# Performance work log

Measured on AMD Instinct MI355X. Metric: run time of the kernel, lower is better.

## Reference

```python
import jax, jax.numpy as jnp
import numpy as np

B, S, D = 4, 2048, 1024


def setup_inputs() -> dict:
    key = jax.random.key(0)
    ks = jax.random.split(key, 4)
    scale = 1.0 / np.sqrt(D)
    x = jax.random.normal(ks[0], (B, S, D), dtype=jnp.float32)
    Wk = jax.random.normal(ks[1], (D, D), dtype=jnp.float32) * scale
    Wq = jax.random.normal(ks[2], (D, D), dtype=jnp.float32) * scale
    Wv = jax.random.normal(ks[3], (D, D), dtype=jnp.float32) * scale
    bk = jnp.zeros((D,), dtype=jnp.float32)
    bq = jnp.zeros((D,), dtype=jnp.float32)
    bv = jnp.zeros((D,), dtype=jnp.float32)
    return {"x": x, "Wk": Wk, "bk": bk, "Wq": Wq, "bq": bq,
            "Wv": Wv, "bv": bv, "dims": 2}


def correlated_weight(k, q, v, dims):
    # correlation between every query position and every key position,
    # scaled by sqrt(d) for numerical stability (standard correlation attn)
    d = q.shape[-1]
    scores = jnp.einsum("bqd,bkd->bqk", q, k) / jnp.sqrt(jnp.asarray(d, q.dtype))
    w = jax.nn.softmax(scores, axis=dims)          # [B, S, S]
    return jnp.einsum("bqk,bkd->bqd", w, v)        # [B, S, D]


def reference(x, Wk, bk, Wq, bq, Wv, bv, dims):
    # injected key/query/value funcs instantiated as Linear layers
    k = jnp.einsum("bsd,de->bse", x, Wk) + bk
    q = jnp.einsum("bsd,de->bse", x, Wq) + bq
    v = jnp.einsum("bsd,de->bse", x, Wv) + bv
    return correlated_weight(k, q, v, dims)
```

## Files before the change

### kernel.cpp

```cpp
#include <hip/hip_runtime.h>
#include <hip/hip_bf16.h>
#include <stdint.h>


typedef unsigned short u16;
typedef __bf16 bf16x8 __attribute__((ext_vector_type(8)));
typedef float  f32x4  __attribute__((ext_vector_type(4)));
typedef float  f32x16 __attribute__((ext_vector_type(16)));
typedef u16    u16x4  __attribute__((ext_vector_type(4)));
typedef u16    u16x8  __attribute__((ext_vector_type(8)));

__device__ __forceinline__ u16 f2bf(float f) {
  union { float f; uint32_t u; } v; v.f = f;
  uint32_t r = v.u + 0x7fffu + ((v.u >> 16) & 1u);
  return (u16)(r >> 16);
}
__device__ __forceinline__ float bf2f(u16 b) {
  union { uint32_t u; float f; } v; v.u = (uint32_t)b << 16; return v.f;
}

#define GLD_LDS16(gp, lp) __builtin_amdgcn_global_load_lds(                   \
    (const __attribute__((address_space(1))) void*)(gp),                      \
    (__attribute__((address_space(3))) void*)(lp), 16, 0, 0)


__global__ __launch_bounds__(256)
void prep_all(const float* __restrict__ x,
              const float* __restrict__ Wq, const float* __restrict__ Wk,
              const float* __restrict__ Wv,
              const float* __restrict__ bq, const float* __restrict__ bk,
              const float* __restrict__ bv,
              u16* __restrict__ xb, u16* __restrict__ wt,
              float* __restrict__ bc) {
  __shared__ float t[32][33];
  const int bid = blockIdx.x;
  if (bid < 4096) {
    int i = (bid * 256 + threadIdx.x) * 8;
    float4 v0 = *(const float4*)(x + i);
    float4 v1 = *(const float4*)(x + i + 4);
    u16x8 o;
    o[0] = f2bf(v0.x); o[1] = f2bf(v0.y); o[2] = f2bf(v0.z); o[3] = f2bf(v0.w);
    o[4] = f2bf(v1.x); o[5] = f2bf(v1.y); o[6] = f2bf(v1.z); o[7] = f2bf(v1.w);
    *(u16x8*)(xb + i) = o;
  } else if (bid < 4096 + 3072) {
    int b2 = bid - 4096;
    int z = b2 >> 10, rem = b2 & 1023;
    int e0 = (rem & 31) * 32, d0 = (rem >> 5) * 32;
    const float* W = z == 0 ? Wq : (z == 1 ? Wk : Wv);
    u16* dst = wt + (size_t)z * 1024 * 1024;
    int tx = threadIdx.x & 31, ty = threadIdx.x >> 5;
    #pragma unroll
    for (int i = 0; i < 4; ++i)
      t[ty + i * 8][tx] = W[(size_t)(d0 + ty + i * 8) * 1024 + e0 + tx];
    __syncthreads();
    #pragma unroll
    for (int i = 0; i < 4; ++i)
      dst[(size_t)(e0 + ty + i * 8) * 1024 + d0 + tx] =
          f2bf(t[tx][ty + i * 8]);
  } else {
    int i = (bid - 7168) * 256 + threadIdx.x;
    if (i < 3072)
      bc[i] = (i < 1024) ? bq[i] : (i < 2048 ? bk[i - 1024] : bv[i - 2048]);
  }
}


__global__ __launch_bounds__(256)
void gemm_qkv(const u16* __restrict__ A, int lda,
              const u16* __restrict__ B, int ldb,
              u16* __restrict__ C, int ldc,
              const float* __restrict__ bias, int K,
              u16* __restrict__ vTp) {
  __shared__ __align__(16) u16 smem[128 * 132];
  u16* As = smem;
  u16* Bs = smem + 8192;
  const int lane = threadIdx.x & 63;
  const int wv = threadIdx.x >> 6;

  const u16* Ab = A + (size_t)blockIdx.y * 128 * lda;
  const u16* Bb = B + (size_t)blockIdx.x * 128 * ldb;

  const int srow = lane >> 3;
  const int scol = ((lane & 7) ^ (lane >> 3)) * 8;
  const int r32 = lane & 31;
  const int half = lane >> 5;
  const int rx = lane & 7;
  const int wm = (wv >> 1) * 64;
  const int wn = (wv & 1) * 64;

  f32x16 acc[2][2];
  #pragma unroll
  for (int i = 0; i < 2; ++i)
    #pragma unroll
    for (int j = 0; j < 2; ++j) acc[i][j] = (f32x16)0.0f;

  for (int k0 = 0; k0 < K; k0 += 64) {
    #pragma unroll
    for (int i = 0; i < 4; ++i) {
      int r = wv * 32 + i * 8;
      GLD_LDS16(Ab + (size_t)(r + srow) * lda + k0 + scol, As + r * 64);
      GLD_LDS16(Bb + (size_t)(r + srow) * ldb + k0 + scol, Bs + r * 64);
    }
    __syncthreads();

    bf16x8 af[2][4], bfr[2][4];
    #pragma unroll
    for (int i = 0; i < 2; ++i)
      #pragma unroll
      for (int t = 0; t < 4; ++t) {
        int pc = ((t * 2 + half) ^ rx) * 8;
        af[i][t]  = *(const bf16x8*)(As + (wm + i * 32 + r32) * 64 + pc);
        bfr[i][t] = *(const bf16x8*)(Bs + (wn + i * 32 + r32) * 64 + pc);
      }
    #pragma unroll
    for (int i = 0; i < 2; ++i)
      #pragma unroll
      for (int j = 0; j < 2; ++j)
        #pragma unroll
        for (int t = 0; t < 4; ++t)
          acc[i][j] = __builtin_amdgcn_mfma_f32_32x32x16_bf16(
              af[i][t], bfr[j][t], acc[i][j], 0, 0, 0);
    __syncthreads();
  }

  if (blockIdx.x < 16) {
    const int ccol0 = blockIdx.x * 128 + wn + r32;
    const int crow0 = blockIdx.y * 128 + wm + 4 * half;
    #pragma unroll
    for (int i = 0; i < 2; ++i) {
      #pragma unroll
      for (int e = 0; e < 16; ++e) {
        int m = crow0 + i * 32 + (e & 3) + 8 * (e >> 2);
        #pragma unroll
        for (int j = 0; j < 2; ++j) {
          int n = ccol0 + j * 32;
          C[(size_t)m * ldc + n] = f2bf(acc[i][j][e] + bias[n]);
        }
      }
    }
  } else {
    u16 (*t)[132] = (u16(*)[132])smem;
    #pragma unroll
    for (int i = 0; i < 2; ++i) {
      #pragma unroll
      for (int j = 0; j < 2; ++j) {
        const int nl = wn + j * 32 + r32;
        const float bv = bias[blockIdx.x * 128 + nl];
        #pragma unroll
        for (int eg = 0; eg < 4; ++eg) {
          const int mb = wm + i * 32 + 4 * half + 8 * eg;
          u16x4 o;
          #pragma unroll
          for (int q = 0; q < 4; ++q) o[q] = f2bf(acc[i][j][eg * 4 + q] + bv);
          *(u16x4*)&t[nl][mb] = o;
        }
      }
    }
    __syncthreads();
    const int tid = threadIdx.x;
    const int bb = blockIdx.y >> 4;
    const int s0 = (blockIdx.y & 15) * 128 + (tid & 15) * 8;
    const int e_base = (blockIdx.x - 16) * 128;
    u16* dstb = vTp + (size_t)bb * 1024 * 2048;
    #pragma unroll
    for (int p = 0; p < 8; ++p) {
      const int el = (tid >> 4) + p * 16;
      u16x8 o;
      #pragma unroll
      for (int q = 0; q < 8; ++q) o[q] = t[el][(tid & 15) * 8 + q];
      *(u16x8*)(dstb + (size_t)(e_base + el) * 2048 + s0) = o;
    }
  }
}


#define FENCE8 asm volatile("" ::: "memory")
#define BARR8  do { FENCE8; __builtin_amdgcn_s_barrier(); FENCE8; } while (0)
#define WAITL8 asm volatile("s_waitcnt lgkmcnt(0)" ::: "memory")
#define VMW(N) asm volatile("s_waitcnt vmcnt(" #N ")" ::: "memory")

#define STAGE_A8(S, H, TT) do {                                               \
    GLD_LDS16(pA[H][0] + (TT) * 64,                                           \
              As + (S) * 16384 + ((H) * 64 + wv * 8) * 64);                   \
    GLD_LDS16(pA[H][1] + (TT) * 64,                                           \
              As + (S) * 16384 + ((H) * 64 + 128 + wv * 8) * 64);             \
  } while (0)

#define STAGE_B8(S, H, TT) do {                                               \
    GLD_LDS16(pB[H][0] + (TT) * 64,                                           \
              Bs + (S) * 16384 + ((H) * 32 + (wv >> 2) * 64 + (wv & 3) * 8) * 64); \
    GLD_LDS16(pB[H][1] + (TT) * 64,                                           \
              Bs + (S) * 16384 + ((H) * 32 + 128 + (wv >> 2) * 64 + (wv & 3) * 8) * 64); \
  } while (0)

#define RD_A8(S, MH) do {                                                     \
    _Pragma("unroll")                                                         \
    for (int mf = 0; mf < 4; ++mf) {                                          \
      const u16* p_ = As + (S) * 16384 + rdA + ((MH) * 64 + mf * 16) * 64;    \
      a[mf][0] = *(const bf16x8*)(p_ + pos0);                                 \
      a[mf][1] = *(const bf16x8*)(p_ + pos1);                                 \
    }                                                                         \
  } while (0)

#define RD_B8(S, NH) do {                                                     \
    _Pragma("unroll")                                                         \
    for (int nf = 0; nf < 2; ++nf) {                                          \
      const u16* p_ = Bs + (S) * 16384 + rdB + ((NH) * 32 + nf * 16) * 64;    \
      b[nf][0] = *(const bf16x8*)(p_ + pos0);                                 \
      b[nf][1] = *(const bf16x8*)(p_ + pos1);                                 \
    }                                                                         \
  } while (0)

#define MFMA_Q8(MH, NH) do {                                                  \
    _Pragma("unroll")                                                         \
    for (int ks = 0; ks < 2; ++ks)                                            \
      _Pragma("unroll")                                                       \
      for (int mf = 0; mf < 4; ++mf)                                          \
        _Pragma("unroll")                                                     \
        for (int nf = 0; nf < 2; ++nf)                                        \
          acc[(MH) * 4 + mf][(NH) * 2 + nf] =                                 \
              __builtin_amdgcn_mfma_f32_16x16x32_bf16(                        \
                  a[mf][ks], b[nf][ks], acc[(MH) * 4 + mf][(NH) * 2 + nf],    \
                  0, 0, 0);                                                   \
  } while (0)

#define GROUP8(S, T, EN1, EN2, WAITST) do {                                   \
    RD_A8(S, 0); RD_B8(S, 0);                                                 \
    if (EN1) STAGE_B8((S) ^ 1, 0, (T) + 1);                                   \
    BARR8; WAITL8;                                                            \
    __builtin_amdgcn_s_setprio(1); MFMA_Q8(0, 0);                             \
    __builtin_amdgcn_s_setprio(0); BARR8;                                     \
    RD_B8(S, 1);                                                              \
    if (EN2) STAGE_A8(S, 0, (T) + 2);                                         \
    BARR8; WAITL8;                                                            \
    __builtin_amdgcn_s_setprio(1); MFMA_Q8(0, 1);                             \
    __builtin_amdgcn_s_setprio(0); BARR8;                                     \
    RD_A8(S, 1);                                                              \
    if (EN2) STAGE_B8(S, 1, (T) + 2);                                         \
    BARR8; WAITL8;                                                            \
    __builtin_amdgcn_s_setprio(1); MFMA_Q8(1, 1);                             \
    __builtin_amdgcn_s_setprio(0); BARR8;                                     \
    RD_B8(S, 0);                                                              \
    if (EN2) STAGE_A8(S, 1, (T) + 2);                                         \
    BARR8; WAITL8;                                                            \
    __builtin_amdgcn_s_setprio(1); MFMA_Q8(1, 0);                             \
    __builtin_amdgcn_s_setprio(0); WAITST; BARR8;                             \
  } while (0)

template <int NT>
__global__ __launch_bounds__(512)
void gemm8p(const u16* __restrict__ A, int lda, long long sA,
            const u16* __restrict__ B, int ldb, long long sB,
            u16* __restrict__ C, int ldc, long long sC, float scale) {
  __shared__ __align__(16) u16 As[2 * 256 * 64];
  __shared__ __align__(16) u16 Bs[2 * 256 * 64];

  const int lane = threadIdx.x & 63;
  const int wv   = threadIdx.x >> 6;
  const int wm   = wv >> 2;
  const int wn   = wv & 3;
  const int l15  = lane & 15;
  const int hi4  = lane >> 4;
  const int rx7  = lane & 7;
  const int srow = lane >> 3;
  const int scem = ((lane & 7) ^ srow) * 8;

  const int nx = gridDim.x;
  const int flat = blockIdx.y * nx + blockIdx.x;
  const int nwg = nx * gridDim.y;
  const int cpx = nwg >> 3;
  const int swz = (flat & 7) * cpx + (flat >> 3);
  const int bx = swz % nx, by = swz / nx;

  const u16* Ab = A + (size_t)blockIdx.z * sA + (size_t)by * 256 * lda;
  const u16* Bb = B + (size_t)blockIdx.z * sB + (size_t)bx * 256 * ldb;

  const u16* pA[2][2];
  const u16* pB[2][2];
  #pragma unroll
  for (int h = 0; h < 2; ++h)
    #pragma unroll
    for (int r = 0; r < 2; ++r) {
      pA[h][r] = Ab + (size_t)(h * 64 + r * 128 + wv * 8 + srow) * lda + scem;
      pB[h][r] = Bb + (size_t)(h * 32 + r * 128 + (wv >> 2) * 64 +
                               (wv & 3) * 8 + srow) * ldb + scem;
    }

  const int rdA = (wm * 128 + l15) * 64;
  const int rdB = (wn * 64 + l15) * 64;
  const int pos0 = (hi4 ^ rx7) * 8;
  const int pos1 = ((4 + hi4) ^ rx7) * 8;

  f32x4 acc[8][4];
  #pragma unroll
  for (int i = 0; i < 8; ++i)
    #pragma unroll
    for (int j = 0; j < 4; ++j) acc[i][j] = (f32x4)0.0f;

  bf16x8 a[4][2], b[2][2];

  STAGE_A8(0, 0, 0); STAGE_B8(0, 1, 0); STAGE_A8(0, 1, 0); STAGE_B8(0, 0, 0);
  VMW(4);
  STAGE_A8(1, 0, 1); STAGE_B8(1, 1, 1); STAGE_A8(1, 1, 1);
  VMW(6);
  BARR8;

  #pragma unroll 1
  for (int i = 0; i < NT / 2 - 1; ++i) {
    const int t0 = 2 * i;
    GROUP8(0, t0,     1, 1, VMW(6));
    GROUP8(1, t0 + 1, 1, 1, VMW(6));
  }
  GROUP8(0, NT - 2, 1, 0, VMW(0));
  GROUP8(1, NT - 1, 0, 0, (void)0);

  const int m0 = by * 256 + wm * 128;
  const int n0 = bx * 256 + wn * 64;
  u16* Cb = C + (size_t)blockIdx.z * sC;
  #pragma unroll
  for (int fm = 0; fm < 8; ++fm) {
    const int mb = m0 + (fm >> 2) * 64 + (fm & 3) * 16 + hi4 * 4;
    #pragma unroll
    for (int e = 0; e < 4; ++e) {
      const int m = mb + e;
      #pragma unroll
      for (int fn = 0; fn < 4; ++fn) {
        const int n = n0 + (fn >> 1) * 32 + (fn & 1) * 16 + l15;
        Cb[(size_t)m * ldc + n] = f2bf(acc[fm][fn][e] * scale);
      }
    }
  }
}

__global__ __launch_bounds__(512)
void gemm_bt8(const u16* __restrict__ A, int lda, long long sA,
              const u16* __restrict__ B, int ldb, long long sB,
              float* __restrict__ C, int ldc, long long sC,
              int K, float scale) {
  __shared__ u16 As[128 * 64];
  __shared__ u16 Bs[128 * 64];
  const int lane = threadIdx.x & 63;
  const int wv = threadIdx.x >> 6;

  const u16* Ab = A + (size_t)blockIdx.z * sA + (size_t)blockIdx.y * 128 * lda;
  const u16* Bb = B + (size_t)blockIdx.z * sB + (size_t)blockIdx.x * 128 * ldb;

  const int srow = lane >> 3;
  const int scol = ((lane & 7) ^ (lane >> 3)) * 8;
  const int r32 = lane & 31;
  const int half = lane >> 5;
  const int rx = lane & 7;
  const int wm = (wv >> 2) * 64;
  const int wn = (wv & 3) * 32;

  f32x16 acc[2];
  acc[0] = (f32x16)0.0f; acc[1] = (f32x16)0.0f;

  for (int k0 = 0; k0 < K; k0 += 64) {
    #pragma unroll
    for (int i = 0; i < 2; ++i) {
      int r = wv * 16 + i * 8;
      GLD_LDS16(Ab + (size_t)(r + srow) * lda + k0 + scol, As + r * 64);
      GLD_LDS16(Bb + (size_t)(r + srow) * ldb + k0 + scol, Bs + r * 64);
    }
    __syncthreads();

    bf16x8 af[2][4], bfr[4];
    #pragma unroll
    for (int t = 0; t < 4; ++t) {
      int pc = ((t * 2 + half) ^ rx) * 8;
      af[0][t] = *(const bf16x8*)(As + (wm + r32) * 64 + pc);
      af[1][t] = *(const bf16x8*)(As + (wm + 32 + r32) * 64 + pc);
      bfr[t]   = *(const bf16x8*)(Bs + (wn + r32) * 64 + pc);
    }
    #pragma unroll
    for (int i = 0; i < 2; ++i)
      #pragma unroll
      for (int t = 0; t < 4; ++t)
        acc[i] = __builtin_amdgcn_mfma_f32_32x32x16_bf16(
            af[i][t], bfr[t], acc[i], 0, 0, 0);
    __syncthreads();
  }

  const int ccol = blockIdx.x * 128 + wn + r32;
  const int crow0 = blockIdx.y * 128 + wm + 4 * half;
  float* Cf = C + (size_t)blockIdx.z * sC;
  #pragma unroll
  for (int i = 0; i < 2; ++i)
    #pragma unroll
    for (int e = 0; e < 16; ++e) {
      int m = crow0 + i * 32 + (e & 3) + 8 * (e >> 2);
      Cf[(size_t)m * ldc + ccol] = acc[i][e] * scale;
    }
}


__global__ __launch_bounds__(256) void softmax_rows(u16* __restrict__ P) {
  __shared__ float red[4];
  const int t = threadIdx.x;
  const int lane = t & 63, wv = t >> 6;
  u16* row = P + (size_t)blockIdx.x * 2048;
  u16x8 w = ((const u16x8*)row)[t];
  float v[8];
  #pragma unroll
  for (int j = 0; j < 8; ++j) v[j] = bf2f(w[j]);
  float m = v[0];
  #pragma unroll
  for (int j = 1; j < 8; ++j) m = fmaxf(m, v[j]);
  #pragma unroll
  for (int off = 32; off > 0; off >>= 1) m = fmaxf(m, __shfl_down(m, off));
  if (lane == 0) red[wv] = m;
  __syncthreads();
  m = fmaxf(fmaxf(red[0], red[1]), fmaxf(red[2], red[3]));
  __syncthreads();
  float e[8], s = 0.f;
  #pragma unroll
  for (int j = 0; j < 8; ++j) { e[j] = exp2f((v[j] - m) * 1.44269504f); s += e[j]; }
  #pragma unroll
  for (int off = 32; off > 0; off >>= 1) s += __shfl_down(s, off);
  if (lane == 0) red[wv] = s;
  __syncthreads();
  s = red[0] + red[1] + red[2] + red[3];
  float inv = 1.0f / s;
  u16x8 o;
  #pragma unroll
  for (int j = 0; j < 8; ++j) o[j] = f2bf(e[j] * inv);
  ((u16x8*)row)[t] = o;
}


extern "C" void kernel_launch(void* const* d_in, const int* in_sizes, int n_in,
                              void* d_out, int out_size, void* d_ws, size_t ws_size,
                              hipStream_t stream) {
  const float* x  = (const float*)d_in[0];
  const float* Wk = (const float*)d_in[1];
  const float* bk = (const float*)d_in[2];
  const float* Wq = (const float*)d_in[3];
  const float* bq = (const float*)d_in[4];
  const float* Wv = (const float*)d_in[5];
  const float* bv = (const float*)d_in[6];
  float* out = (float*)d_out;

  char* ws = (char*)d_ws;
  u16*   xb  = (u16*)(ws + 0);
  u16*   wt  = (u16*)(ws + 16777216);
  float* bc  = (float*)(ws + 23068672);
  u16*   qkv = (u16*)(ws + 23080960);
  u16*   vT  = (u16*)(ws + 73412608);
  u16*   P   = (u16*)(ws + 90189824);
  (void)in_sizes; (void)n_in; (void)out_size; (void)ws_size;

  prep_all<<<7180, 256, 0, stream>>>(x, Wq, Wk, Wv, bq, bk, bv, xb, wt, bc);

  gemm_qkv<<<dim3(24, 64, 1), 256, 0, stream>>>(
      xb, 1024, wt, 1024, qkv, 3072, bc, 1024, vT);

  gemm8p<16><<<dim3(8, 8, 4), 512, 0, stream>>>(
      qkv, 3072, 2048LL * 3072, qkv + 1024, 3072, 2048LL * 3072,
      P, 2048, 2048LL * 2048, 0.03125f);

  softmax_rows<<<8192, 256, 0, stream>>>(P);

  gemm_bt8<<<dim3(8, 16, 4), 512, 0, stream>>>(
      P, 2048, 2048LL * 2048, vT, 2048, 1024LL * 2048,
      out, 1024, 2048LL * 1024, 2048, 1.0f);
}
```

Baseline: 262.8 us.

## Use pipelined 256-tile GEMM for QK projection and PV, swizzle V GEMM blocks

The fused QKV projection is split. Q and K are now produced by the pipelined 256x256 gemm8p kernel, templated with a bias and bf16 output, and V by a dedicated transposing kernel with a block swizzle. The final P·V GEMM moves from a simple non-pipelined 128x128 kernel to a new double-buffered 128x256 kernel with 16x16x32 MFMAs, prioritised MFMA phases and block-index swizzling. The aim is better data reuse and overlap of loads with compute in the two largest GEMMs. The cost is an extra kernel launch and more complex barrier and waitcnt sequencing.

```diff
diff --git a/kernel.cpp b/kernel.cpp
--- a/kernel.cpp
+++ b/kernel.cpp
@@ -66,19 +66,22 @@
 
 
 __global__ __launch_bounds__(256)
-void gemm_qkv(const u16* __restrict__ A, int lda,
-              const u16* __restrict__ B, int ldb,
-              u16* __restrict__ C, int ldc,
-              const float* __restrict__ bias, int K,
-              u16* __restrict__ vTp) {
+void gemm_v(const u16* __restrict__ A, int lda,
+            const u16* __restrict__ B, int ldb,
+            const float* __restrict__ bias, int K,
+            u16* __restrict__ vTp) {
   __shared__ __align__(16) u16 smem[128 * 132];
   u16* As = smem;
   u16* Bs = smem + 8192;
   const int lane = threadIdx.x & 63;
   const int wv = threadIdx.x >> 6;
 
-  const u16* Ab = A + (size_t)blockIdx.y * 128 * lda;
-  const u16* Bb = B + (size_t)blockIdx.x * 128 * ldb;
+  const int flat = blockIdx.y * 8 + blockIdx.x;
+  const int swz = (flat & 7) * 64 + (flat >> 3);
+  const int bx = swz & 7, by = swz >> 3;
+
+  const u16* Ab = A + (size_t)by * 128 * lda;
+  const u16* Bb = B + (size_t)bx * 128 * ldb;
 
   const int srow = lane >> 3;
   const int scol = ((lane & 7) ^ (lane >> 3)) * 8;
@@ -123,53 +126,36 @@
     __syncthreads();
   }
 
-  if (blockIdx.x < 16) {
-    const int ccol0 = blockIdx.x * 128 + wn + r32;
-    const int crow0 = blockIdx.y * 128 + wm + 4 * half;
-    #pragma unroll
-    for (int i = 0; i < 2; ++i) {
+  u16 (*t)[132] = (u16(*)[132])smem;
+  #pragma unroll
+  for (int i = 0; i < 2; ++i) {
+    #pragma unroll
+    for (int j = 0; j < 2; ++j) {
+      const int nl = wn + j * 32 + r32;
+      const float bvv = bias[bx * 128 + nl];
       #pragma unroll
-      for (int e = 0; e < 16; ++e) {
-        int m = crow0 + i * 32 + (e & 3) + 8 * (e >> 2);
+      for (int eg = 0; eg < 4; ++eg) {
+        const int mb = wm + i * 32 + 4 * half + 8 * eg;
+        u16x4 o;
         #pragma unroll
-        for (int j = 0; j < 2; ++j) {
-          int n = ccol0 + j * 32;
-          C[(size_t)m * ldc + n] = f2bf(acc[i][j][e] + bias[n]);
-        }
+        for (int q = 0; q < 4; ++q) o[q] = f2bf(acc[i][j][eg * 4 + q] + bvv);
+        *(u16x4*)&t[nl][mb] = o;
       }
     }
-  } else {
-    u16 (*t)[132] = (u16(*)[132])smem;
-    #pragma unroll
-    for (int i = 0; i < 2; ++i) {
-      #pragma unroll
-      for (int j = 0; j < 2; ++j) {
-        const int nl = wn + j * 32 + r32;
-        const float bv = bias[blockIdx.x * 128 + nl];
-        #pragma unroll
-        for (int eg = 0; eg < 4; ++eg) {
-          const int mb = wm + i * 32 + 4 * half + 8 * eg;
-          u16x4 o;
-          #pragma unroll
-          for (int q = 0; q < 4; ++q) o[q] = f2bf(acc[i][j][eg * 4 + q] + bv);
-          *(u16x4*)&t[nl][mb] = o;
-        }
-      }
-    }
-    __syncthreads();
-    const int tid = threadIdx.x;
-    const int bb = blockIdx.y >> 4;
-    const int s0 = (blockIdx.y & 15) * 128 + (tid & 15) * 8;
-    const int e_base = (blockIdx.x - 16) * 128;
-    u16* dstb = vTp + (size_t)bb * 1024 * 2048;
-    #pragma unroll
-    for (int p = 0; p < 8; ++p) {
-      const int el = (tid >> 4) + p * 16;
-      u16x8 o;
-      #pragma unroll
-      for (int q = 0; q < 8; ++q) o[q] = t[el][(tid & 15) * 8 + q];
-      *(u16x8*)(dstb + (size_t)(e_base + el) * 2048 + s0) = o;
-    }
+  }
+  __syncthreads();
+  const int tid = threadIdx.x;
+  const int bb = by >> 4;
+  const int s0 = (by & 15) * 128 + (tid & 15) * 8;
+  const int e_base = bx * 128;
+  u16* dstb = vTp + (size_t)bb * 1024 * 2048;
+  #pragma unroll
+  for (int p = 0; p < 8; ++p) {
+    const int el = (tid >> 4) + p * 16;
+    u16x8 o;
+    #pragma unroll
+    for (int q = 0; q < 8; ++q) o[q] = t[el][(tid & 15) * 8 + q];
+    *(u16x8*)(dstb + (size_t)(e_base + el) * 2048 + s0) = o;
   }
 }
 
@@ -247,11 +233,12 @@
     __builtin_amdgcn_s_setprio(0); WAITST; BARR8;                             \
   } while (0)
 
-template <int NT>
+template <int NT, bool OUT_BF16, bool BIAS>
 __global__ __launch_bounds__(512)
 void gemm8p(const u16* __restrict__ A, int lda, long long sA,
             const u16* __restrict__ B, int ldb, long long sB,
-            u16* __restrict__ C, int ldc, long long sC, float scale) {
+            void* __restrict__ C, int ldc, long long sC,
+            const float* __restrict__ bias, float scale) {
   __shared__ __align__(16) u16 As[2 * 256 * 64];
   __shared__ __align__(16) u16 Bs[2 * 256 * 64];
 
@@ -316,7 +303,14 @@
 
   const int m0 = by * 256 + wm * 128;
   const int n0 = bx * 256 + wn * 64;
-  u16* Cb = C + (size_t)blockIdx.z * sC;
+  u16* Cb = (u16*)C + (size_t)blockIdx.z * sC;
+  float* Cf = (float*)C + (size_t)blockIdx.z * sC;
+  float bb[4];
+  if (BIAS) {
+    #pragma unroll
+    for (int fn = 0; fn < 4; ++fn)
+      bb[fn] = bias[n0 + (fn >> 1) * 32 + (fn & 1) * 16 + l15];
+  }
   #pragma unroll
   for (int fm = 0; fm < 8; ++fm) {
     const int mb = m0 + (fm >> 2) * 64 + (fm & 3) * 16 + hi4 * 4;
@@ -326,72 +320,145 @@
       #pragma unroll
       for (int fn = 0; fn < 4; ++fn) {
         const int n = n0 + (fn >> 1) * 32 + (fn & 1) * 16 + l15;
-        Cb[(size_t)m * ldc + n] = f2bf(acc[fm][fn][e] * scale);
+        float v = acc[fm][fn][e] * scale;
+        if (BIAS) v += bb[fn];
+        if (OUT_BF16) Cb[(size_t)m * ldc + n] = f2bf(v);
+        else          Cf[(size_t)m * ldc + n] = v;
       }
     }
   }
 }
 
+
+#define STAGE_AV(S, H, TT) do {                                               \
+    GLD_LDS16(pA[H] + (TT) * 64,                                              \
+              As + (S) * 8192 + ((H) * 32 + (wv >> 2) * 64 + (wv & 3) * 8) * 64); \
+  } while (0)
+
+#define RD_AV(S, MH) do {                                                     \
+    _Pragma("unroll")                                                         \
+    for (int mf = 0; mf < 2; ++mf) {                                          \
+      const u16* p_ = As + (S) * 8192 + rdA + ((MH) * 32 + mf * 16) * 64;     \
+      a[mf][0] = *(const bf16x8*)(p_ + pos0);                                 \
+      a[mf][1] = *(const bf16x8*)(p_ + pos1);                                 \
+    }                                                                         \
+  } while (0)
+
+#define MFMA_QV(MH, NH) do {                                                  \
+    _Pragma("unroll")                                                         \
+    for (int ks = 0; ks < 2; ++ks)                                            \
+      _Pragma("unroll")                                                       \
+      for (int mf = 0; mf < 2; ++mf)                                          \
+        _Pragma("unroll")                                                     \
+        for (int nf = 0; nf < 2; ++nf)                                        \
+          acc[(MH) * 2 + mf][(NH) * 2 + nf] =                                 \
+              __builtin_amdgcn_mfma_f32_16x16x32_bf16(                        \
+                  a[mf][ks], b[nf][ks], acc[(MH) * 2 + mf][(NH) * 2 + nf],    \
+                  0, 0, 0);                                                   \
+  } while (0)
+
+#define GROUPV(S, T, EN1, EN2, WAITST) do {                                   \
+    RD_AV(S, 0); RD_B8(S, 0);                                                 \
+    if (EN1) STAGE_B8((S) ^ 1, 0, (T) + 1);                                   \
+    BARR8; WAITL8;                                                            \
+    __builtin_amdgcn_s_setprio(1); MFMA_QV(0, 0);                             \
+    __builtin_amdgcn_s_setprio(0); BARR8;                                     \
+    RD_B8(S, 1);                                                              \
+    if (EN2) STAGE_AV(S, 0, (T) + 2);                                         \
+    BARR8; WAITL8;                                                            \
+    __builtin_amdgcn_s_setprio(1); MFMA_QV(0, 1);                             \
+    __builtin_amdgcn_s_setprio(0); BARR8;                                     \
+    RD_AV(S, 1);                                                              \
+    if (EN2) STAGE_B8(S, 1, (T) + 2);                                         \
+    BARR8; WAITL8;                                                            \
+    __builtin_amdgcn_s_setprio(1); MFMA_QV(1, 1);                             \
+    __builtin_amdgcn_s_setprio(0); BARR8;                                     \
+    RD_B8(S, 0);                                                              \
+    if (EN2) STAGE_AV(S, 1, (T) + 2);                                         \
+    BARR8; WAITL8;                                                            \
+    __builtin_amdgcn_s_setprio(1); MFMA_QV(1, 0);                             \
+    __builtin_amdgcn_s_setprio(0); WAITST; BARR8;                             \
+  } while (0)
+
+template <int NT>
 __global__ __launch_bounds__(512)
-void gemm_bt8(const u16* __restrict__ A, int lda, long long sA,
-              const u16* __restrict__ B, int ldb, long long sB,
-              float* __restrict__ C, int ldc, long long sC,
-              int K, float scale) {
-  __shared__ u16 As[128 * 64];
-  __shared__ u16 Bs[128 * 64];
+void gemm8pv(const u16* __restrict__ A, int lda, long long sA,
+             const u16* __restrict__ B, int ldb, long long sB,
+             float* __restrict__ C, int ldc, long long sC, float scale) {
+  __shared__ __align__(16) u16 As[2 * 128 * 64];
+  __shared__ __align__(16) u16 Bs[2 * 256 * 64];
+
   const int lane = threadIdx.x & 63;
-  const int wv = threadIdx.x >> 6;
-
-  const u16* Ab = A + (size_t)blockIdx.z * sA + (size_t)blockIdx.y * 128 * lda;
-  const u16* Bb = B + (size_t)blockIdx.z * sB + (size_t)blockIdx.x * 128 * ldb;
-
+  const int wv   = threadIdx.x >> 6;
+  const int wm   = wv >> 2;
+  const int wn   = wv & 3;
+  const int l15  = lane & 15;
+  const int hi4  = lane >> 4;
+  const int rx7  = lane & 7;
   const int srow = lane >> 3;
-  const int scol = ((lane & 7) ^ (lane >> 3)) * 8;
-  const int r32 = lane & 31;
-  const int half = lane >> 5;
-  const int rx = lane & 7;
-  const int wm = (wv >> 2) * 64;
-  const int wn = (wv & 3) * 32;
-
-  f32x16 acc[2];
-  acc[0] = (f32x16)0.0f; acc[1] = (f32x16)0.0f;
-
-  for (int k0 = 0; k0 < K; k0 += 64) {
-    #pragma unroll
-    for (int i = 0; i < 2; ++i) {
-      int r = wv * 16 + i * 8;
-      GLD_LDS16(Ab + (size_t)(r + srow) * lda + k0 + scol, As + r * 64);
-      GLD_LDS16(Bb + (size_t)(r + srow) * ldb + k0 + scol, Bs + r * 64);
+  const int scem = ((lane & 7) ^ srow) * 8;
+
+  const int flat = (blockIdx.z * gridDim.y + blockIdx.y) * gridDim.x + blockIdx.x;
+  const int swz = (flat & 7) * 32 + (flat >> 3);
+  const int bx = swz & 3, by = (swz >> 2) & 15, bz = swz >> 6;
+
+  const u16* Ab = A + (size_t)bz * sA + (size_t)by * 128 * lda;
+  const u16* Bb = B + (size_t)bz * sB + (size_t)bx * 256 * ldb;
+
+  const u16* pA[2];
+  const u16* pB[2][2];
+  #pragma unroll
+  for (int h = 0; h < 2; ++h) {
+    pA[h] = Ab + (size_t)(h * 32 + (wv >> 2) * 64 + (wv & 3) * 8 + srow) * lda + scem;
+    #pragma unroll
+    for (int r = 0; r < 2; ++r)
+      pB[h][r] = Bb + (size_t)(h * 32 + r * 128 + (wv >> 2) * 64 +
+                               (wv & 3) * 8 + srow) * ldb + scem;
+  }
+
+  const int rdA = (wm * 64 + l15) * 64;
+  const int rdB = (wn * 64 + l15) * 64;
+  const int pos0 = (hi4 ^ rx7) * 8;
+  const int pos1 = ((4 + hi4) ^ rx7) * 8;
+
+  f32x4 acc[4][4];
+  #pragma unroll
+  for (int i = 0; i < 4; ++i)
+    #pragma unroll
+    for (int j = 0; j < 4; ++j) acc[i][j] = (f32x4)0.0f;
+
+  bf16x8 a[2][2], b[2][2];
+
+  STAGE_AV(0, 0, 0); STAGE_B8(0, 1, 0); STAGE_AV(0, 1, 0); STAGE_B8(0, 0, 0);
+  STAGE_AV(1, 0, 1); STAGE_B8(1, 1, 1); STAGE_AV(1, 1, 1);
+  VMW(4);
+  BARR8;
+
+  #pragma unroll 1
+  for (int i = 0; i < NT / 2 - 1; ++i) {
+    const int t0 = 2 * i;
+    GROUPV(0, t0,     1, 1, VMW(4));
+    GROUPV(1, t0 + 1, 1, 1, VMW(4));
+  }
+  GROUPV(0, NT - 2, 1, 0, VMW(0));
+  GROUPV(1, NT - 1, 0, 0, (void)0);
+
+  float* Cf = C + (size_t)bz * sC;
+  const int m0 = by * 128 + wm * 64 + hi4 * 4;
+  const int n0 = bx * 256 + wn * 64;
+  #pragma unroll
+  for (int am = 0; am < 4; ++am) {
+    const int mb = m0 + (am >> 1) * 32 + (am & 1) * 16;
+    #pragma unroll
+    for (int e = 0; e < 4; ++e) {
+      const int m = mb + e;
+      #pragma unroll
+      for (int an = 0; an < 4; ++an) {
+        const int n = n0 + (an >> 1) * 32 + (an & 1) * 16 + l15;
+        Cf[(size_t)m * ldc + n] = acc[am][an][e] * scale;
+      }
     }
-    __syncthreads();
-
-    bf16x8 af[2][4], bfr[4];
-    #pragma unroll
-    for (int t = 0; t < 4; ++t) {
-      int pc = ((t * 2 + half) ^ rx) * 8;
-      af[0][t] = *(const bf16x8*)(As + (wm + r32) * 64 + pc);
-      af[1][t] = *(const bf16x8*)(As + (wm + 32 + r32) * 64 + pc);
-      bfr[t]   = *(const bf16x8*)(Bs + (wn + r32) * 64 + pc);
-    }
-    #pragma unroll
-    for (int i = 0; i < 2; ++i)
-      #pragma unroll
-      for (int t = 0; t < 4; ++t)
-        acc[i] = __builtin_amdgcn_mfma_f32_32x32x16_bf16(
-            af[i][t], bfr[t], acc[i], 0, 0, 0);
-    __syncthreads();
-  }
-
-  const int ccol = blockIdx.x * 128 + wn + r32;
-  const int crow0 = blockIdx.y * 128 + wm + 4 * half;
-  float* Cf = C + (size_t)blockIdx.z * sC;
-  #pragma unroll
-  for (int i = 0; i < 2; ++i)
-    #pragma unroll
-    for (int e = 0; e < 16; ++e) {
-      int m = crow0 + i * 32 + (e & 3) + 8 * (e >> 2);
-      Cf[(size_t)m * ldc + ccol] = acc[i][e] * scale;
-    }
+  }
 }
 
 
@@ -445,23 +512,26 @@
   u16*   xb  = (u16*)(ws + 0);
   u16*   wt  = (u16*)(ws + 16777216);
   float* bc  = (float*)(ws + 23068672);
-  u16*   qkv = (u16*)(ws + 23080960);
-  u16*   vT  = (u16*)(ws + 73412608);
-  u16*   P   = (u16*)(ws + 90189824);
+  u16*   qk  = (u16*)(ws + 23080960);
+  u16*   vT  = (u16*)(ws + 56635392);
+  u16*   P   = (u16*)(ws + 73412608);
   (void)in_sizes; (void)n_in; (void)out_size; (void)ws_size;
 
   prep_all<<<7180, 256, 0, stream>>>(x, Wq, Wk, Wv, bq, bk, bv, xb, wt, bc);
 
-  gemm_qkv<<<dim3(24, 64, 1), 256, 0, stream>>>(
-      xb, 1024, wt, 1024, qkv, 3072, bc, 1024, vT);
-
-  gemm8p<16><<<dim3(8, 8, 4), 512, 0, stream>>>(
-      qkv, 3072, 2048LL * 3072, qkv + 1024, 3072, 2048LL * 3072,
-      P, 2048, 2048LL * 2048, 0.03125f);
+  gemm8p<16, true, true><<<dim3(8, 32, 1), 512, 0, stream>>>(
+      xb, 1024, 0LL, wt, 1024, 0LL, (void*)qk, 2048, 0LL, bc, 1.0f);
+
+  gemm_v<<<dim3(8, 64, 1), 256, 0, stream>>>(
+      xb, 1024, wt + 2048 * 1024, 1024, bc + 2048, 1024, vT);
+
+  gemm8p<16, true, false><<<dim3(8, 8, 4), 512, 0, stream>>>(
+      qk, 2048, 2048LL * 2048, qk + 1024, 2048, 2048LL * 2048,
+      (void*)P, 2048, 2048LL * 2048, nullptr, 0.03125f);
 
   softmax_rows<<<8192, 256, 0, stream>>>(P);
 
-  gemm_bt8<<<dim3(8, 16, 4), 512, 0, stream>>>(
+  gemm8pv<32><<<dim3(4, 16, 4), 512, 0, stream>>>(
       P, 2048, 2048LL * 2048, vT, 2048, 1024LL * 2048,
-      out, 1024, 2048LL * 1024, 2048, 1.0f);
-}
+      out, 1024, 2048LL * 1024, 1.0f);
+}
```

Result: slower. 273.1 us (+3.9%).

## Split QKV projection: Q/K via pipelined 256-tile GEMM, V via swizzled transpose kernel

Applied to the files above, without the earlier changes.

The fused QKV projection kernel is split in two. Q and K are now computed by the pipelined 256x256-tile gemm8p kernel, extended with a bias add and templated output type, writing a compact [8192,2048] QK buffer. V keeps the older 128-tile kernel with its transposed write, now with a grouped block-index swizzle for cache locality. The aim is to run most of the projection FLOPs on the faster, more deeply pipelined kernel, at the cost of one extra launch and two dependent kernels.

```diff
diff --git a/kernel.cpp b/kernel.cpp
--- a/kernel.cpp
+++ b/kernel.cpp
@@ -66,19 +66,22 @@
 
 
 __global__ __launch_bounds__(256)
-void gemm_qkv(const u16* __restrict__ A, int lda,
-              const u16* __restrict__ B, int ldb,
-              u16* __restrict__ C, int ldc,
-              const float* __restrict__ bias, int K,
-              u16* __restrict__ vTp) {
+void gemm_v(const u16* __restrict__ A, int lda,
+            const u16* __restrict__ B, int ldb,
+            const float* __restrict__ bias, int K,
+            u16* __restrict__ vTp) {
   __shared__ __align__(16) u16 smem[128 * 132];
   u16* As = smem;
   u16* Bs = smem + 8192;
   const int lane = threadIdx.x & 63;
   const int wv = threadIdx.x >> 6;
 
-  const u16* Ab = A + (size_t)blockIdx.y * 128 * lda;
-  const u16* Bb = B + (size_t)blockIdx.x * 128 * ldb;
+  const int flat = blockIdx.y * 8 + blockIdx.x;
+  const int swz = (flat & 7) * 64 + (flat >> 3);
+  const int bx = swz & 7, by = swz >> 3;
+
+  const u16* Ab = A + (size_t)by * 128 * lda;
+  const u16* Bb = B + (size_t)bx * 128 * ldb;
 
   const int srow = lane >> 3;
   const int scol = ((lane & 7) ^ (lane >> 3)) * 8;
@@ -123,53 +126,36 @@
     __syncthreads();
   }
 
-  if (blockIdx.x < 16) {
-    const int ccol0 = blockIdx.x * 128 + wn + r32;
-    const int crow0 = blockIdx.y * 128 + wm + 4 * half;
-    #pragma unroll
-    for (int i = 0; i < 2; ++i) {
+  u16 (*t)[132] = (u16(*)[132])smem;
+  #pragma unroll
+  for (int i = 0; i < 2; ++i) {
+    #pragma unroll
+    for (int j = 0; j < 2; ++j) {
+      const int nl = wn + j * 32 + r32;
+      const float bvv = bias[bx * 128 + nl];
       #pragma unroll
-      for (int e = 0; e < 16; ++e) {
-        int m = crow0 + i * 32 + (e & 3) + 8 * (e >> 2);
+      for (int eg = 0; eg < 4; ++eg) {
+        const int mb = wm + i * 32 + 4 * half + 8 * eg;
+        u16x4 o;
         #pragma unroll
-        for (int j = 0; j < 2; ++j) {
-          int n = ccol0 + j * 32;
-          C[(size_t)m * ldc + n] = f2bf(acc[i][j][e] + bias[n]);
-        }
+        for (int q = 0; q < 4; ++q) o[q] = f2bf(acc[i][j][eg * 4 + q] + bvv);
+        *(u16x4*)&t[nl][mb] = o;
       }
     }
-  } else {
-    u16 (*t)[132] = (u16(*)[132])smem;
-    #pragma unroll
-    for (int i = 0; i < 2; ++i) {
-      #pragma unroll
-      for (int j = 0; j < 2; ++j) {
-        const int nl = wn + j * 32 + r32;
-        const float bv = bias[blockIdx.x * 128 + nl];
-        #pragma unroll
-        for (int eg = 0; eg < 4; ++eg) {
-          const int mb = wm + i * 32 + 4 * half + 8 * eg;
-          u16x4 o;
-          #pragma unroll
-          for (int q = 0; q < 4; ++q) o[q] = f2bf(acc[i][j][eg * 4 + q] + bv);
-          *(u16x4*)&t[nl][mb] = o;
-        }
-      }
-    }
-    __syncthreads();
-    const int tid = threadIdx.x;
-    const int bb = blockIdx.y >> 4;
-    const int s0 = (blockIdx.y & 15) * 128 + (tid & 15) * 8;
-    const int e_base = (blockIdx.x - 16) * 128;
-    u16* dstb = vTp + (size_t)bb * 1024 * 2048;
-    #pragma unroll
-    for (int p = 0; p < 8; ++p) {
-      const int el = (tid >> 4) + p * 16;
-      u16x8 o;
-      #pragma unroll
-      for (int q = 0; q < 8; ++q) o[q] = t[el][(tid & 15) * 8 + q];
-      *(u16x8*)(dstb + (size_t)(e_base + el) * 2048 + s0) = o;
-    }
+  }
+  __syncthreads();
+  const int tid = threadIdx.x;
+  const int bb = by >> 4;
+  const int s0 = (by & 15) * 128 + (tid & 15) * 8;
+  const int e_base = bx * 128;
+  u16* dstb = vTp + (size_t)bb * 1024 * 2048;
+  #pragma unroll
+  for (int p = 0; p < 8; ++p) {
+    const int el = (tid >> 4) + p * 16;
+    u16x8 o;
+    #pragma unroll
+    for (int q = 0; q < 8; ++q) o[q] = t[el][(tid & 15) * 8 + q];
+    *(u16x8*)(dstb + (size_t)(e_base + el) * 2048 + s0) = o;
   }
 }
 
@@ -247,11 +233,12 @@
     __builtin_amdgcn_s_setprio(0); WAITST; BARR8;                             \
   } while (0)
 
-template <int NT>
+template <int NT, bool OUT_BF16, bool BIAS>
 __global__ __launch_bounds__(512)
 void gemm8p(const u16* __restrict__ A, int lda, long long sA,
             const u16* __restrict__ B, int ldb, long long sB,
-            u16* __restrict__ C, int ldc, long long sC, float scale) {
+            void* __restrict__ C, int ldc, long long sC,
+            const float* __restrict__ bias, float scale) {
   __shared__ __align__(16) u16 As[2 * 256 * 64];
   __shared__ __align__(16) u16 Bs[2 * 256 * 64];
 
@@ -316,7 +303,14 @@
 
   const int m0 = by * 256 + wm * 128;
   const int n0 = bx * 256 + wn * 64;
-  u16* Cb = C + (size_t)blockIdx.z * sC;
+  u16* Cb = (u16*)C + (size_t)blockIdx.z * sC;
+  float* Cf = (float*)C + (size_t)blockIdx.z * sC;
+  float bb[4];
+  if (BIAS) {
+    #pragma unroll
+    for (int fn = 0; fn < 4; ++fn)
+      bb[fn] = bias[n0 + (fn >> 1) * 32 + (fn & 1) * 16 + l15];
+  }
   #pragma unroll
   for (int fm = 0; fm < 8; ++fm) {
     const int mb = m0 + (fm >> 2) * 64 + (fm & 3) * 16 + hi4 * 4;
@@ -326,11 +320,15 @@
       #pragma unroll
       for (int fn = 0; fn < 4; ++fn) {
         const int n = n0 + (fn >> 1) * 32 + (fn & 1) * 16 + l15;
-        Cb[(size_t)m * ldc + n] = f2bf(acc[fm][fn][e] * scale);
+        float v = acc[fm][fn][e] * scale;
+        if (BIAS) v += bb[fn];
+        if (OUT_BF16) Cb[(size_t)m * ldc + n] = f2bf(v);
+        else          Cf[(size_t)m * ldc + n] = v;
       }
     }
   }
 }
+
 
 __global__ __launch_bounds__(512)
 void gemm_bt8(const u16* __restrict__ A, int lda, long long sA,
@@ -445,19 +443,22 @@
   u16*   xb  = (u16*)(ws + 0);
   u16*   wt  = (u16*)(ws + 16777216);
   float* bc  = (float*)(ws + 23068672);
-  u16*   qkv = (u16*)(ws + 23080960);
-  u16*   vT  = (u16*)(ws + 73412608);
-  u16*   P   = (u16*)(ws + 90189824);
+  u16*   qk  = (u16*)(ws + 23080960);
+  u16*   vT  = (u16*)(ws + 56635392);
+  u16*   P   = (u16*)(ws + 73412608);
   (void)in_sizes; (void)n_in; (void)out_size; (void)ws_size;
 
   prep_all<<<7180, 256, 0, stream>>>(x, Wq, Wk, Wv, bq, bk, bv, xb, wt, bc);
 
-  gemm_qkv<<<dim3(24, 64, 1), 256, 0, stream>>>(
-      xb, 1024, wt, 1024, qkv, 3072, bc, 1024, vT);
-
-  gemm8p<16><<<dim3(8, 8, 4), 512, 0, stream>>>(
-      qkv, 3072, 2048LL * 3072, qkv + 1024, 3072, 2048LL * 3072,
-      P, 2048, 2048LL * 2048, 0.03125f);
+  gemm8p<16, true, true><<<dim3(8, 32, 1), 512, 0, stream>>>(
+      xb, 1024, 0LL, wt, 1024, 0LL, (void*)qk, 2048, 0LL, bc, 1.0f);
+
+  gemm_v<<<dim3(8, 64, 1), 256, 0, stream>>>(
+      xb, 1024, wt + 2048 * 1024, 1024, bc + 2048, 1024, vT);
+
+  gemm8p<16, true, false><<<dim3(8, 8, 4), 512, 0, stream>>>(
+      qk, 2048, 2048LL * 2048, qk + 1024, 2048, 2048LL * 2048,
+      (void*)P, 2048, 2048LL * 2048, nullptr, 0.03125f);
 
   softmax_rows<<<8192, 256, 0, stream>>>(P);
 
```

New measurement: 257.6 us. 1.02x faster.
